# Kernel optimization log

Hardware: AMD Instinct MI355X
Metric: run time of the kernel (lower is better)

Reference implementation:

```python
import jax, jax.numpy as jnp
import numpy as np

GRID_SIZE = 128  # D = H = W
N_POINTS = 8388608


def setup_inputs() -> dict:
    key = jax.random.key(0)
    k_grid, k_coords = jax.random.split(key)
    # occupancy grid buffer: binary {0,1} values as float, shape [D, H, W]
    grid = (jax.random.uniform(k_grid, (GRID_SIZE, GRID_SIZE, GRID_SIZE)) > 0.5).astype(jnp.float32)
    # normalized [-1, 1] query coordinates, layout [..., 3] = (x, y, z)
    coords = jax.random.uniform(k_coords, (N_POINTS, 3), minval=-1.0, maxval=1.0, dtype=jnp.float32)
    return {"grid": grid, "coords": coords}


def _trilinear_sample(grid, coords):
    """torch.nn.functional.grid_sample 5D, mode='bilinear', align_corners=False,
    padding_mode='zeros'. grid: [D,H,W]; coords: [N,3] with (x,y,z) where
    x indexes W, y indexes H, z indexes D. Returns [N]."""
    D, H, W = grid.shape
    x, y, z = coords[:, 0], coords[:, 1], coords[:, 2]
    # unnormalize (align_corners=False): pixel = ((c + 1) * size - 1) / 2
    ix = ((x + 1.0) * W - 1.0) * 0.5
    iy = ((y + 1.0) * H - 1.0) * 0.5
    iz = ((z + 1.0) * D - 1.0) * 0.5

    ix0 = jnp.floor(ix)
    iy0 = jnp.floor(iy)
    iz0 = jnp.floor(iz)
    wx = ix - ix0  # fractional weights
    wy = iy - iy0
    wz = iz - iz0
    ix0 = ix0.astype(jnp.int32)
    iy0 = iy0.astype(jnp.int32)
    iz0 = iz0.astype(jnp.int32)

    def gather(zi, yi, xi):
        # zero padding: out-of-bounds corners contribute 0
        valid = ((zi >= 0) & (zi < D) & (yi >= 0) & (yi < H) & (xi >= 0) & (xi < W))
        zc = jnp.clip(zi, 0, D - 1)
        yc = jnp.clip(yi, 0, H - 1)
        xc = jnp.clip(xi, 0, W - 1)
        return jnp.where(valid, grid[zc, yc, xc], 0.0)

    out = (
        gather(iz0,     iy0,     ix0    ) * (1 - wz) * (1 - wy) * (1 - wx)
        + gather(iz0,     iy0,     ix0 + 1) * (1 - wz) * (1 - wy) * wx
        + gather(iz0,     iy0 + 1, ix0    ) * (1 - wz) * wy       * (1 - wx)
        + gather(iz0,     iy0 + 1, ix0 + 1) * (1 - wz) * wy       * wx
        + gather(iz0 + 1, iy0,     ix0    ) * wz       * (1 - wy) * (1 - wx)
        + gather(iz0 + 1, iy0,     ix0 + 1) * wz       * (1 - wy) * wx
        + gather(iz0 + 1, iy0 + 1, ix0    ) * wz       * wy       * (1 - wx)
        + gather(iz0 + 1, iy0 + 1, ix0 + 1) * wz       * wy       * wx
    )
    return out


def reference(grid, coords):
    flat = coords.reshape(-1, 3)
    return _trilinear_sample(grid, flat)
```

## Files before the change

kernel.cpp:

```cpp
#include <hip/hip_runtime.h>


typedef float fx4 __attribute__((ext_vector_type(4)));
typedef unsigned int u32;
typedef unsigned int ux4 __attribute__((ext_vector_type(4)));
typedef unsigned long long u64;

constexpr int GS = 128;
constexpr size_t MASK_BYTES = (size_t)GS * GS * GS / 8;
constexpr int SLAB_WORDS = 33281;
constexpr size_t SLAB_LDS = (size_t)SLAB_WORDS * 4;

constexpr int TD = GS + 1;
constexpr size_t TBL_BYTES = (size_t)TD * TD * TD;
constexpr size_t TBL_OFF   = (MASK_BYTES + 63) & ~(size_t)63;
constexpr size_t WS_FB     = TBL_OFF + TBL_BYTES;

__global__ __launch_bounds__(256)
void bitpack_kernel(const float* __restrict__ grid, u64* __restrict__ mask) {
    int gid = blockIdx.x * blockDim.x + threadIdx.x;
    float v = grid[gid];
    u64 m = __ballot(v != 0.0f);
    if ((threadIdx.x & 63) == 0) mask[gid >> 6] = m;
}

__device__ __forceinline__ unsigned bit_at(u64 lo, u64 hi, int xi) {
    if ((unsigned)xi >= 128u) return 0u;
    u64 w = (xi < 64) ? lo : hi;
    return (unsigned)((w >> (xi & 63)) & 1ull);
}

__global__ __launch_bounds__(256)
void table_kernel(const u64* __restrict__ mask, unsigned char* __restrict__ tbl) {
    int i = blockIdx.x * blockDim.x + threadIdx.x;
    if (i >= (int)TBL_BYTES) return;
    int x = i % TD;
    int t = i / TD;
    int y = t % TD;
    int z = t / TD;
    int x0 = x - 1;
    unsigned byte = 0u;
#pragma unroll
    for (int dz = 0; dz < 2; ++dz) {
#pragma unroll
        for (int dy = 0; dy < 2; ++dy) {
            int yi = y - 1 + dy, zi = z - 1 + dz;
            u64 lo = 0ull, hi = 0ull;
            if (((unsigned)yi < 128u) & ((unsigned)zi < 128u)) {
                int r = (zi * 128 + yi) * 2;
                lo = mask[r];
                hi = mask[r + 1];
            }
            int kk = dy * 2 + dz * 4;
            byte |= (bit_at(lo, hi, x0) << kk) | (bit_at(lo, hi, x0 + 1) << (kk + 1));
        }
    }
    tbl[i] = (unsigned char)byte;
}

__global__ __launch_bounds__(256)
void sample_packed(const unsigned char* __restrict__ tbl,
                   const float* __restrict__ coords,
                   float* __restrict__ out, int nt) {
    int t = blockIdx.x * blockDim.x + threadIdx.x;
    if (t >= nt) return;
    const fx4* c4 = (const fx4*)coords;
    fx4 q[6];
#pragma unroll
    for (int j = 0; j < 6; ++j) q[j] = __builtin_nontemporal_load(&c4[6 * t + j]);
    const float* f = (const float*)q;
    float wxa[8], wya[8], wza[8];
    int addr[8];
#pragma unroll
    for (int i = 0; i < 8; ++i) {
        float ix = fmaf(f[3 * i + 0], 64.0f, 63.5f);
        float iy = fmaf(f[3 * i + 1], 64.0f, 63.5f);
        float iz = fmaf(f[3 * i + 2], 64.0f, 63.5f);
        float fx = floorf(ix), fy = floorf(iy), fz = floorf(iz);
        wxa[i] = ix - fx; wya[i] = iy - fy; wza[i] = iz - fz;
        int xb = (int)fx + 1, yb = (int)fy + 1, zb = (int)fz + 1;
        addr[i] = (zb * TD + yb) * TD + xb;
    }
    unsigned bytes[8];
#pragma unroll
    for (int i = 0; i < 8; ++i) bytes[i] = (unsigned)tbl[addr[i]];
    float o[8];
#pragma unroll
    for (int i = 0; i < 8; ++i) {
        unsigned byte = bytes[i];
        float wx = wxa[i], wy = wya[i], wz = wza[i];
        float v0 = (float)( byte       & 1u);
        float v1 = (float)((byte >> 1) & 1u);
        float v2 = (float)((byte >> 2) & 1u);
        float v3 = (float)((byte >> 3) & 1u);
        float v4 = (float)((byte >> 4) & 1u);
        float v5 = (float)((byte >> 5) & 1u);
        float v6 = (float)((byte >> 6) & 1u);
        float v7 = (float)((byte >> 7) & 1u);
        float c00 = v0 + wx * (v1 - v0);
        float c10 = v2 + wx * (v3 - v2);
        float c01 = v4 + wx * (v5 - v4);
        float c11 = v6 + wx * (v7 - v6);
        float c0  = c00 + wy * (c10 - c00);
        float c1  = c01 + wy * (c11 - c01);
        o[i] = c0 + wz * (c1 - c0);
    }
    fx4* o4 = (fx4*)out;
    fx4 r0 = {o[0], o[1], o[2], o[3]};
    fx4 r1 = {o[4], o[5], o[6], o[7]};
    __builtin_nontemporal_store(r0, &o4[2 * t + 0]);
    __builtin_nontemporal_store(r1, &o4[2 * t + 1]);
}

__global__ __launch_bounds__(1024, 4)
void sample_2p(const u32* __restrict__ mask32,
               const float* __restrict__ coords,
               float* __restrict__ out) {
    extern __shared__ u32 lds[];
    const int tid = threadIdx.x;
    const int T = blockIdx.x * 1024 + tid;
    const fx4* c4 = (const fx4*)coords;
    fx4 q[6];
#pragma unroll
    for (int j = 0; j < 6; ++j) q[j] = c4[6 * T + j];
    const float* f = (const float*)q;

    u32 pack1[8];
    u32 AM = 0;
    float wx[8], wy[8], wz[8], o[8];
#pragma unroll
    for (int j = 0; j < 8; ++j) {
        float ix = fmaf(f[3 * j + 0], 64.0f, 63.5f);
        float iy = fmaf(f[3 * j + 1], 64.0f, 63.5f);
        float iz = fmaf(f[3 * j + 2], 64.0f, 63.5f);
        float fx = floorf(ix), fy = floorf(iy), fz = floorf(iz);
        float w0 = ix - fx;
        wy[j] = iy - fy; wz[j] = iz - fz;
        int x0 = (int)fx, y0 = (int)fy, z0 = (int)fz;
        int zb = z0 + 1;
        bool flip = (x0 < 0);
        wx[j] = flip ? 1.0f - w0 : w0;
        int xc = flip ? 0 : x0;
        int sft = xc & 31;
        u32 xm = ((u32)x0 <= 126u) ? 3u : 1u;
        u32 vy0 = (u32)(y0 >= 0);
        u32 vy1 = (u32)((u32)y0 <= 126u);
        u32 a0 = vy0 ? xm : 0u;
        u32 a1 = vy1 ? xm : 0u;
        u32 am = a0 | (a1 << 2);
        u32 dyf = vy0 & vy1;
        int y0c = y0 < 0 ? 0 : y0;
        int z0c = z0 < 0 ? 0 : z0;
        u32 RA = (u32)(((z0c << 7) + y0c) * 4 + (xc >> 5));
        pack1[j] = RA | ((u32)sft << 16) | ((u32)zb << 21) | (dyf << 29);
        AM |= am << (4 * j);
        o[j] = 0.0f;
    }

#pragma unroll 1
    for (int s = 0; s < 2; ++s) {
        const int base_w = s ? 32256 : 0;
        const int nv4    = s ? 8320 : 8192;
        __syncthreads();
        {
            const ux4* src = (const ux4*)(mask32 + base_w);
            ux4* dst = (ux4*)lds;
            for (int i = tid; i < nv4; i += 1024) dst[i] = src[i];
            if (s && tid == 0) lds[33280] = 0;
        }
        __syncthreads();
#pragma unroll
        for (int j = 0; j < 8; ++j) {
            u32 p1 = pack1[j];
            int zb = (int)((p1 >> 21) & 0xFF);
            if ((zb < 64) != (s == 0)) continue;
            int la  = (int)(p1 & 0xFFFF) - base_w;
            int sft = (int)((p1 >> 16) & 31);
            int dyw = (int)((p1 >> 27) & 4);
            bool edge = s ? (zb == 128) : (zb == 0);
            int dz = edge ? 0 : 512;
            u32 amv = (AM >> (4 * j)) & 15u;
            u32 glo = amv, ghi = amv;
            if (s) ghi = edge ? 0u : amv;
            else   glo = edge ? 0u : amv;
            int l0 = la, l1 = la + dyw, l2 = la + dz, l3 = la + dz + dyw;
            u32 w00 = lds[l0], w01 = lds[l0 + 1];
            u32 w10 = lds[l1], w11 = lds[l1 + 1];
            u32 w20 = lds[l2], w21 = lds[l2 + 1];
            u32 w30 = lds[l3], w31 = lds[l3 + 1];
            u32 t0 = __builtin_amdgcn_alignbit(w01, w00, (u32)sft) & (glo & 3u);
            u32 t1 = __builtin_amdgcn_alignbit(w11, w10, (u32)sft) & ((glo >> 2) & 3u);
            u32 t2 = __builtin_amdgcn_alignbit(w21, w20, (u32)sft) & (ghi & 3u);
            u32 t3 = __builtin_amdgcn_alignbit(w31, w30, (u32)sft) & ((ghi >> 2) & 3u);
            float w = wx[j];
            int b0 = (int)(t0 & 1u), b1 = (int)(t1 & 1u);
            int b2 = (int)(t2 & 1u), b3 = (int)(t3 & 1u);
            float r00 = fmaf(w, (float)((int)(t0 >> 1) - b0), (float)b0);
            float r01 = fmaf(w, (float)((int)(t1 >> 1) - b1), (float)b1);
            float r10 = fmaf(w, (float)((int)(t2 >> 1) - b2), (float)b2);
            float r11 = fmaf(w, (float)((int)(t3 >> 1) - b3), (float)b3);
            float cy0 = fmaf(wy[j], r01 - r00, r00);
            float cy1 = fmaf(wy[j], r11 - r10, r10);
            o[j] = fmaf(wz[j], cy1 - cy0, cy0);
        }
    }
    fx4* o4 = (fx4*)out;
    fx4 r0 = {o[0], o[1], o[2], o[3]};
    fx4 r1 = {o[4], o[5], o[6], o[7]};
    o4[2 * T]     = r0;
    o4[2 * T + 1] = r1;
}

extern "C" void kernel_launch(void* const* d_in, const int* in_sizes, int n_in,
                              void* d_out, int out_size, void* d_ws, size_t ws_size,
                              hipStream_t stream) {
    const float* grid   = (const float*)d_in[0];
    const float* coords = (const float*)d_in[1];
    float* out = (float*)d_out;
    int npts = in_sizes[1] / 3;
    int vox = GS * GS * GS;

    u64* mask = (u64*)d_ws;

    if (ws_size >= WS_FB && (npts & 7) == 0) {
        unsigned char* tbl = (unsigned char*)d_ws + TBL_OFF;
        bitpack_kernel<<<vox / 256, 256, 0, stream>>>(grid, mask);
        table_kernel<<<(int)((TBL_BYTES + 255) / 256), 256, 0, stream>>>(mask, tbl);
        int nt = npts / 8;
        sample_packed<<<(nt + 255) / 256, 256, 0, stream>>>(tbl, coords, out, nt);
        return;
    }

    (void)hipFuncSetAttribute((const void*)sample_2p,
                              hipFuncAttributeMaxDynamicSharedMemorySize,
                              (int)SLAB_LDS);
    int nb = 0;
    hipError_t oe = hipOccupancyMaxActiveBlocksPerMultiprocessor(
        &nb, sample_2p, 1024, SLAB_LDS);
    bool slab_ok = (oe == hipSuccess) && (nb >= 1) && (ws_size >= MASK_BYTES) &&
                   (npts == 1024 * 8192);
    if (slab_ok) {
        bitpack_kernel<<<vox / 256, 256, 0, stream>>>(grid, mask);
        sample_2p<<<1024, 1024, SLAB_LDS, stream>>>((const u32*)mask, coords, out);
    }
}
```

Measured before the change: 216.8 us.

## Split points between LDS-slab path and global byte-table path in one hybrid kernel

```diff
diff --git a/kernel.cpp b/kernel.cpp
--- a/kernel.cpp
+++ b/kernel.cpp
@@ -15,6 +15,9 @@
 constexpr size_t TBL_BYTES = (size_t)TD * TD * TD;
 constexpr size_t TBL_OFF   = (MASK_BYTES + 63) & ~(size_t)63;
 constexpr size_t WS_FB     = TBL_OFF + TBL_BYTES;
+
+constexpr int NPTS_FULL = 8388608;
+constexpr int HGRP = NPTS_FULL / 2 / 8;
 
 __global__ __launch_bounds__(256)
 void bitpack_kernel(const float* __restrict__ grid, u64* __restrict__ mask) {
@@ -58,72 +61,24 @@
     tbl[i] = (unsigned char)byte;
 }
 
-__global__ __launch_bounds__(256)
-void sample_packed(const unsigned char* __restrict__ tbl,
+__global__ __launch_bounds__(1024, 4)
+void sample_hybrid(const u32* __restrict__ mask32,
+                   const unsigned char* __restrict__ tbl,
                    const float* __restrict__ coords,
-                   float* __restrict__ out, int nt) {
-    int t = blockIdx.x * blockDim.x + threadIdx.x;
-    if (t >= nt) return;
-    const fx4* c4 = (const fx4*)coords;
-    fx4 q[6];
-#pragma unroll
-    for (int j = 0; j < 6; ++j) q[j] = __builtin_nontemporal_load(&c4[6 * t + j]);
-    const float* f = (const float*)q;
-    float wxa[8], wya[8], wza[8];
-    int addr[8];
-#pragma unroll
-    for (int i = 0; i < 8; ++i) {
-        float ix = fmaf(f[3 * i + 0], 64.0f, 63.5f);
-        float iy = fmaf(f[3 * i + 1], 64.0f, 63.5f);
-        float iz = fmaf(f[3 * i + 2], 64.0f, 63.5f);
-        float fx = floorf(ix), fy = floorf(iy), fz = floorf(iz);
-        wxa[i] = ix - fx; wya[i] = iy - fy; wza[i] = iz - fz;
-        int xb = (int)fx + 1, yb = (int)fy + 1, zb = (int)fz + 1;
-        addr[i] = (zb * TD + yb) * TD + xb;
-    }
-    unsigned bytes[8];
-#pragma unroll
-    for (int i = 0; i < 8; ++i) bytes[i] = (unsigned)tbl[addr[i]];
-    float o[8];
-#pragma unroll
-    for (int i = 0; i < 8; ++i) {
-        unsigned byte = bytes[i];
-        float wx = wxa[i], wy = wya[i], wz = wza[i];
-        float v0 = (float)( byte       & 1u);
-        float v1 = (float)((byte >> 1) & 1u);
-        float v2 = (float)((byte >> 2) & 1u);
-        float v3 = (float)((byte >> 3) & 1u);
-        float v4 = (float)((byte >> 4) & 1u);
-        float v5 = (float)((byte >> 5) & 1u);
-        float v6 = (float)((byte >> 6) & 1u);
-        float v7 = (float)((byte >> 7) & 1u);
-        float c00 = v0 + wx * (v1 - v0);
-        float c10 = v2 + wx * (v3 - v2);
-        float c01 = v4 + wx * (v5 - v4);
-        float c11 = v6 + wx * (v7 - v6);
-        float c0  = c00 + wy * (c10 - c00);
-        float c1  = c01 + wy * (c11 - c01);
-        o[i] = c0 + wz * (c1 - c0);
-    }
-    fx4* o4 = (fx4*)out;
-    fx4 r0 = {o[0], o[1], o[2], o[3]};
-    fx4 r1 = {o[4], o[5], o[6], o[7]};
-    __builtin_nontemporal_store(r0, &o4[2 * t + 0]);
-    __builtin_nontemporal_store(r1, &o4[2 * t + 1]);
-}
-
-__global__ __launch_bounds__(1024, 4)
-void sample_2p(const u32* __restrict__ mask32,
-               const float* __restrict__ coords,
-               float* __restrict__ out) {
+                   float* __restrict__ out) {
     extern __shared__ u32 lds[];
     const int tid = threadIdx.x;
-    const int T = blockIdx.x * 1024 + tid;
+    const int Ts = blockIdx.x * 1024 + tid;
+    const int Tg = Ts + HGRP;
     const fx4* c4 = (const fx4*)coords;
-    fx4 q[6];
-#pragma unroll
-    for (int j = 0; j < 6; ++j) q[j] = c4[6 * T + j];
-    const float* f = (const float*)q;
+
+    fx4 qs[6], qg[6];
+#pragma unroll
+    for (int j = 0; j < 6; ++j) qs[j] = __builtin_nontemporal_load(&c4[6 * Ts + j]);
+#pragma unroll
+    for (int j = 0; j < 6; ++j) qg[j] = __builtin_nontemporal_load(&c4[6 * Tg + j]);
+    const float* f  = (const float*)qs;
+    const float* fg = (const float*)qg;
 
     u32 pack1[8];
     u32 AM = 0;
@@ -157,18 +112,42 @@
         o[j] = 0.0f;
     }
 
-#pragma unroll 1
+    u32 gb[8];
+
+#pragma unroll
     for (int s = 0; s < 2; ++s) {
         const int base_w = s ? 32256 : 0;
-        const int nv4    = s ? 8320 : 8192;
-        __syncthreads();
-        {
-            const ux4* src = (const ux4*)(mask32 + base_w);
-            ux4* dst = (ux4*)lds;
-            for (int i = tid; i < nv4; i += 1024) dst[i] = src[i];
-            if (s && tid == 0) lds[33280] = 0;
-        }
-        __syncthreads();
+        if (s) {
+            asm volatile("s_waitcnt lgkmcnt(0)" ::: "memory");
+            __builtin_amdgcn_s_barrier();
+        }
+        const ux4* src = (const ux4*)(mask32 + base_w);
+        ux4* dst4 = (ux4*)lds;
+        ux4 t0 = src[tid], t1 = src[tid + 1024], t2 = src[tid + 2048], t3 = src[tid + 3072];
+        ux4 tt = {0, 0, 0, 0};
+        if (s && tid < 128) tt = src[8192 + tid];
+        dst4[tid] = t0; dst4[tid + 1024] = t1; dst4[tid + 2048] = t2; dst4[tid + 3072] = t3;
+        if (s && tid < 128) dst4[8192 + tid] = tt;
+        ux4 t4 = src[tid + 4096], t5 = src[tid + 5120], t6 = src[tid + 6144], t7 = src[tid + 7168];
+        asm volatile("" ::: "memory");
+#pragma unroll
+        for (int i = 0; i < 4; ++i) {
+            const int p = 4 * s + i;
+            float ix = fmaf(fg[3 * p + 0], 64.0f, 63.5f);
+            float iy = fmaf(fg[3 * p + 1], 64.0f, 63.5f);
+            float iz = fmaf(fg[3 * p + 2], 64.0f, 63.5f);
+            int xb = (int)floorf(ix) + 1;
+            int yb = (int)floorf(iy) + 1;
+            int zb = (int)floorf(iz) + 1;
+            gb[p] = (u32)tbl[(zb * TD + yb) * TD + xb];
+        }
+        asm volatile("" ::: "memory");
+        dst4[tid + 4096] = t4; dst4[tid + 5120] = t5;
+        dst4[tid + 6144] = t6; dst4[tid + 7168] = t7;
+        if (s && tid == 0) lds[33280] = 0;
+        asm volatile("s_waitcnt lgkmcnt(0)" ::: "memory");
+        __builtin_amdgcn_s_barrier();
+
 #pragma unroll
         for (int j = 0; j < 8; ++j) {
             u32 p1 = pack1[j];
@@ -188,27 +167,112 @@
             u32 w10 = lds[l1], w11 = lds[l1 + 1];
             u32 w20 = lds[l2], w21 = lds[l2 + 1];
             u32 w30 = lds[l3], w31 = lds[l3 + 1];
-            u32 t0 = __builtin_amdgcn_alignbit(w01, w00, (u32)sft) & (glo & 3u);
-            u32 t1 = __builtin_amdgcn_alignbit(w11, w10, (u32)sft) & ((glo >> 2) & 3u);
-            u32 t2 = __builtin_amdgcn_alignbit(w21, w20, (u32)sft) & (ghi & 3u);
-            u32 t3 = __builtin_amdgcn_alignbit(w31, w30, (u32)sft) & ((ghi >> 2) & 3u);
+            u32 t0b = __builtin_amdgcn_alignbit(w01, w00, (u32)sft) & (glo & 3u);
+            u32 t1b = __builtin_amdgcn_alignbit(w11, w10, (u32)sft) & ((glo >> 2) & 3u);
+            u32 t2b = __builtin_amdgcn_alignbit(w21, w20, (u32)sft) & (ghi & 3u);
+            u32 t3b = __builtin_amdgcn_alignbit(w31, w30, (u32)sft) & ((ghi >> 2) & 3u);
             float w = wx[j];
-            int b0 = (int)(t0 & 1u), b1 = (int)(t1 & 1u);
-            int b2 = (int)(t2 & 1u), b3 = (int)(t3 & 1u);
-            float r00 = fmaf(w, (float)((int)(t0 >> 1) - b0), (float)b0);
-            float r01 = fmaf(w, (float)((int)(t1 >> 1) - b1), (float)b1);
-            float r10 = fmaf(w, (float)((int)(t2 >> 1) - b2), (float)b2);
-            float r11 = fmaf(w, (float)((int)(t3 >> 1) - b3), (float)b3);
+            int b0 = (int)(t0b & 1u), b1 = (int)(t1b & 1u);
+            int b2 = (int)(t2b & 1u), b3 = (int)(t3b & 1u);
+            float r00 = fmaf(w, (float)((int)(t0b >> 1) - b0), (float)b0);
+            float r01 = fmaf(w, (float)((int)(t1b >> 1) - b1), (float)b1);
+            float r10 = fmaf(w, (float)((int)(t2b >> 1) - b2), (float)b2);
+            float r11 = fmaf(w, (float)((int)(t3b >> 1) - b3), (float)b3);
             float cy0 = fmaf(wy[j], r01 - r00, r00);
             float cy1 = fmaf(wy[j], r11 - r10, r10);
             o[j] = fmaf(wz[j], cy1 - cy0, cy0);
         }
     }
+
+    float og[8];
+#pragma unroll
+    for (int i = 0; i < 8; ++i) {
+        float ix = fmaf(fg[3 * i + 0], 64.0f, 63.5f);
+        float iy = fmaf(fg[3 * i + 1], 64.0f, 63.5f);
+        float iz = fmaf(fg[3 * i + 2], 64.0f, 63.5f);
+        float fx = floorf(ix), fy = floorf(iy), fz = floorf(iz);
+        float gwx = ix - fx, gwy = iy - fy, gwz = iz - fz;
+        unsigned byte = gb[i];
+        float v0 = (float)( byte       & 1u);
+        float v1 = (float)((byte >> 1) & 1u);
+        float v2 = (float)((byte >> 2) & 1u);
+        float v3 = (float)((byte >> 3) & 1u);
+        float v4 = (float)((byte >> 4) & 1u);
+        float v5 = (float)((byte >> 5) & 1u);
+        float v6 = (float)((byte >> 6) & 1u);
+        float v7 = (float)((byte >> 7) & 1u);
+        float c00 = v0 + gwx * (v1 - v0);
+        float c10 = v2 + gwx * (v3 - v2);
+        float c01 = v4 + gwx * (v5 - v4);
+        float c11 = v6 + gwx * (v7 - v6);
+        float c0  = c00 + gwy * (c10 - c00);
+        float c1  = c01 + gwy * (c11 - c01);
+        og[i] = c0 + gwz * (c1 - c0);
+    }
+
     fx4* o4 = (fx4*)out;
     fx4 r0 = {o[0], o[1], o[2], o[3]};
     fx4 r1 = {o[4], o[5], o[6], o[7]};
-    o4[2 * T]     = r0;
-    o4[2 * T + 1] = r1;
+    fx4 g0 = {og[0], og[1], og[2], og[3]};
+    fx4 g1 = {og[4], og[5], og[6], og[7]};
+    __builtin_nontemporal_store(r0, &o4[2 * Ts]);
+    __builtin_nontemporal_store(r1, &o4[2 * Ts + 1]);
+    __builtin_nontemporal_store(g0, &o4[2 * Tg]);
+    __builtin_nontemporal_store(g1, &o4[2 * Tg + 1]);
+}
+
+__global__ __launch_bounds__(256)
+void sample_packed(const unsigned char* __restrict__ tbl,
+                   const float* __restrict__ coords,
+                   float* __restrict__ out, int nt) {
+    int t = blockIdx.x * blockDim.x + threadIdx.x;
+    if (t >= nt) return;
+    const fx4* c4 = (const fx4*)coords;
+    fx4 q[6];
+#pragma unroll
+    for (int j = 0; j < 6; ++j) q[j] = __builtin_nontemporal_load(&c4[6 * t + j]);
+    const float* f = (const float*)q;
+    float wxa[8], wya[8], wza[8];
+    int addr[8];
+#pragma unroll
+    for (int i = 0; i < 8; ++i) {
+        float ix = fmaf(f[3 * i + 0], 64.0f, 63.5f);
+        float iy = fmaf(f[3 * i + 1], 64.0f, 63.5f);
+        float iz = fmaf(f[3 * i + 2], 64.0f, 63.5f);
+        float fx = floorf(ix), fy = floorf(iy), fz = floorf(iz);
+        wxa[i] = ix - fx; wya[i] = iy - fy; wza[i] = iz - fz;
+        int xb = (int)fx + 1, yb = (int)fy + 1, zb = (int)fz + 1;
+        addr[i] = (zb * TD + yb) * TD + xb;
+    }
+    unsigned bytes[8];
+#pragma unroll
+    for (int i = 0; i < 8; ++i) bytes[i] = (unsigned)tbl[addr[i]];
+    float o[8];
+#pragma unroll
+    for (int i = 0; i < 8; ++i) {
+        unsigned byte = bytes[i];
+        float wx = wxa[i], wy = wya[i], wz = wza[i];
+        float v0 = (float)( byte       & 1u);
+        float v1 = (float)((byte >> 1) & 1u);
+        float v2 = (float)((byte >> 2) & 1u);
+        float v3 = (float)((byte >> 3) & 1u);
+        float v4 = (float)((byte >> 4) & 1u);
+        float v5 = (float)((byte >> 5) & 1u);
+        float v6 = (float)((byte >> 6) & 1u);
+        float v7 = (float)((byte >> 7) & 1u);
+        float c00 = v0 + wx * (v1 - v0);
+        float c10 = v2 + wx * (v3 - v2);
+        float c01 = v4 + wx * (v5 - v4);
+        float c11 = v6 + wx * (v7 - v6);
+        float c0  = c00 + wy * (c10 - c00);
+        float c1  = c01 + wy * (c11 - c01);
+        o[i] = c0 + wz * (c1 - c0);
+    }
+    fx4* o4 = (fx4*)out;
+    fx4 r0 = {o[0], o[1], o[2], o[3]};
+    fx4 r1 = {o[4], o[5], o[6], o[7]};
+    __builtin_nontemporal_store(r0, &o4[2 * t + 0]);
+    __builtin_nontemporal_store(r1, &o4[2 * t + 1]);
 }
 
 extern "C" void kernel_launch(void* const* d_in, const int* in_sizes, int n_in,
@@ -222,25 +286,31 @@
 
     u64* mask = (u64*)d_ws;
 
+    if (ws_size >= WS_FB && npts == NPTS_FULL) {
+        (void)hipFuncSetAttribute((const void*)sample_hybrid,
+                                  hipFuncAttributeMaxDynamicSharedMemorySize,
+                                  (int)SLAB_LDS);
+        int nb = 0;
+        hipError_t oe = hipOccupancyMaxActiveBlocksPerMultiprocessor(
+            &nb, sample_hybrid, 1024, SLAB_LDS);
+        unsigned char* tbl = (unsigned char*)d_ws + TBL_OFF;
+        bitpack_kernel<<<vox / 256, 256, 0, stream>>>(grid, mask);
+        table_kernel<<<(int)((TBL_BYTES + 255) / 256), 256, 0, stream>>>(mask, tbl);
+        if (oe == hipSuccess && nb >= 1) {
+            sample_hybrid<<<512, 1024, SLAB_LDS, stream>>>(
+                (const u32*)mask, tbl, coords, out);
+        } else {
+            int nt = npts / 8;
+            sample_packed<<<(nt + 255) / 256, 256, 0, stream>>>(tbl, coords, out, nt);
+        }
+        return;
+    }
+
     if (ws_size >= WS_FB && (npts & 7) == 0) {
         unsigned char* tbl = (unsigned char*)d_ws + TBL_OFF;
         bitpack_kernel<<<vox / 256, 256, 0, stream>>>(grid, mask);
         table_kernel<<<(int)((TBL_BYTES + 255) / 256), 256, 0, stream>>>(mask, tbl);
         int nt = npts / 8;
         sample_packed<<<(nt + 255) / 256, 256, 0, stream>>>(tbl, coords, out, nt);
-        return;
-    }
-
-    (void)hipFuncSetAttribute((const void*)sample_2p,
-                              hipFuncAttributeMaxDynamicSharedMemorySize,
-                              (int)SLAB_LDS);
-    int nb = 0;
-    hipError_t oe = hipOccupancyMaxActiveBlocksPerMultiprocessor(
-        &nb, sample_2p, 1024, SLAB_LDS);
-    bool slab_ok = (oe == hipSuccess) && (nb >= 1) && (ws_size >= MASK_BYTES) &&
-                   (npts == 1024 * 8192);
-    if (slab_ok) {
-        bitpack_kernel<<<vox / 256, 256, 0, stream>>>(grid, mask);
-        sample_2p<<<1024, 1024, SLAB_LDS, stream>>>((const u32*)mask, coords, out);
-    }
-}
+    }
+}
```

Result: no change. 215.0 us (-0.9%).

## Split sample work between LDS-slab waves and table-gather waves; fuse prep kernels

Applied to the files above, without the earlier changes.

```diff
diff --git a/kernel.cpp b/kernel.cpp
--- a/kernel.cpp
+++ b/kernel.cpp
@@ -15,6 +15,9 @@
 constexpr size_t TBL_BYTES = (size_t)TD * TD * TD;
 constexpr size_t TBL_OFF   = (MASK_BYTES + 63) & ~(size_t)63;
 constexpr size_t WS_FB     = TBL_OFF + TBL_BYTES;
+
+constexpr int NPTS_FULL = 8388608;
+constexpr int HGRP = NPTS_FULL / 2 / 8;
 
 __global__ __launch_bounds__(256)
 void bitpack_kernel(const float* __restrict__ grid, u64* __restrict__ mask) {
@@ -31,31 +34,206 @@
 }
 
 __global__ __launch_bounds__(256)
-void table_kernel(const u64* __restrict__ mask, unsigned char* __restrict__ tbl) {
-    int i = blockIdx.x * blockDim.x + threadIdx.x;
-    if (i >= (int)TBL_BYTES) return;
-    int x = i % TD;
-    int t = i / TD;
-    int y = t % TD;
-    int z = t / TD;
-    int x0 = x - 1;
-    unsigned byte = 0u;
-#pragma unroll
-    for (int dz = 0; dz < 2; ++dz) {
-#pragma unroll
-        for (int dy = 0; dy < 2; ++dy) {
-            int yi = y - 1 + dy, zi = z - 1 + dz;
-            u64 lo = 0ull, hi = 0ull;
-            if (((unsigned)yi < 128u) & ((unsigned)zi < 128u)) {
-                int r = (zi * 128 + yi) * 2;
-                lo = mask[r];
-                hi = mask[r + 1];
+void prep_kernel(const float* __restrict__ grid, u64* __restrict__ mask,
+                 unsigned char* __restrict__ tbl) {
+    __shared__ u64 bits[2][256];
+    const int tid = threadIdx.x;
+    const int b = blockIdx.x;
+    const int wid = tid >> 6;
+#pragma unroll
+    for (int p = 0; p < 2; ++p) {
+        int z = b - 1 + p;
+        if ((unsigned)z < 128u) {
+            for (int it = 0; it < 64; ++it) {
+                float v = grid[z * 16384 + it * 256 + tid];
+                u64 m = __ballot(v != 0.0f);
+                if ((tid & 63) == 0) bits[p][it * 4 + wid] = m;
             }
-            int kk = dy * 2 + dz * 4;
-            byte |= (bit_at(lo, hi, x0) << kk) | (bit_at(lo, hi, x0 + 1) << (kk + 1));
-        }
-    }
-    tbl[i] = (unsigned char)byte;
+        } else {
+            bits[p][tid] = 0ull;
+        }
+    }
+    __syncthreads();
+    if (b < 128) mask[b * 256 + tid] = bits[1][tid];
+    for (int i = tid; i < TD * TD; i += 256) {
+        int yb = i / TD, xb = i - yb * TD;
+        int x0 = xb - 1;
+        unsigned byte = 0u;
+#pragma unroll
+        for (int p = 0; p < 2; ++p) {
+#pragma unroll
+            for (int dy = 0; dy < 2; ++dy) {
+                int y = yb - 1 + dy;
+                u64 lo = 0ull, hi = 0ull;
+                if ((unsigned)y < 128u) { lo = bits[p][y * 2]; hi = bits[p][y * 2 + 1]; }
+                int kk = dy * 2 + p * 4;
+                byte |= (bit_at(lo, hi, x0) << kk) | (bit_at(lo, hi, x0 + 1) << (kk + 1));
+            }
+        }
+        tbl[b * (TD * TD) + i] = (unsigned char)byte;
+    }
+}
+
+__global__ __attribute__((amdgpu_waves_per_eu(4, 4))) __launch_bounds__(1024)
+void sample_ws(const u32* __restrict__ mask32,
+               const unsigned char* __restrict__ tbl,
+               const float* __restrict__ coords,
+               float* __restrict__ out) {
+    extern __shared__ u32 lds[];
+    const int tid = threadIdx.x;
+    const bool slab = tid < 512;
+    const int T = blockIdx.x * 512 + (slab ? tid : (HGRP - 512 + tid));
+    const fx4* c4 = (const fx4*)coords;
+
+    fx4 q[6];
+#pragma unroll
+    for (int j = 0; j < 6; ++j) q[j] = __builtin_nontemporal_load(&c4[6 * T + j]);
+    const float* f = (const float*)q;
+
+    float wx[8], wy[8], wz[8], o[8];
+    u32 p1[8];
+    u32 gb[8];
+    u32 AM = 0;
+
+    if (slab) {
+#pragma unroll
+        for (int j = 0; j < 8; ++j) {
+            float ix = fmaf(f[3 * j + 0], 64.0f, 63.5f);
+            float iy = fmaf(f[3 * j + 1], 64.0f, 63.5f);
+            float iz = fmaf(f[3 * j + 2], 64.0f, 63.5f);
+            float fx = floorf(ix), fy = floorf(iy), fz = floorf(iz);
+            float w0 = ix - fx;
+            wy[j] = iy - fy; wz[j] = iz - fz;
+            int x0 = (int)fx, y0 = (int)fy, z0 = (int)fz;
+            int zb = z0 + 1;
+            bool flip = (x0 < 0);
+            wx[j] = flip ? 1.0f - w0 : w0;
+            int xc = flip ? 0 : x0;
+            int sft = xc & 31;
+            u32 xm = ((u32)x0 <= 126u) ? 3u : 1u;
+            u32 vy0 = (u32)(y0 >= 0);
+            u32 vy1 = (u32)((u32)y0 <= 126u);
+            u32 a0 = vy0 ? xm : 0u;
+            u32 a1 = vy1 ? xm : 0u;
+            u32 am = a0 | (a1 << 2);
+            u32 dyf = vy0 & vy1;
+            int y0c = y0 < 0 ? 0 : y0;
+            int z0c = z0 < 0 ? 0 : z0;
+            u32 RA = (u32)(((z0c << 7) + y0c) * 4 + (xc >> 5));
+            p1[j] = RA | ((u32)sft << 16) | ((u32)zb << 21) | (dyf << 29);
+            AM |= am << (4 * j);
+            o[j] = 0.0f;
+        }
+    } else {
+#pragma unroll
+        for (int i = 0; i < 8; ++i) {
+            float ix = fmaf(f[3 * i + 0], 64.0f, 63.5f);
+            float iy = fmaf(f[3 * i + 1], 64.0f, 63.5f);
+            float iz = fmaf(f[3 * i + 2], 64.0f, 63.5f);
+            float fx = floorf(ix), fy = floorf(iy), fz = floorf(iz);
+            wx[i] = ix - fx; wy[i] = iy - fy; wz[i] = iz - fz;
+            int xb = (int)fx + 1, yb = (int)fy + 1, zb = (int)fz + 1;
+            p1[i] = (u32)((zb * TD + yb) * TD + xb);
+        }
+#pragma unroll
+        for (int i = 0; i < 4; ++i) gb[i] = (u32)tbl[p1[i]];
+    }
+
+    auto fill = [&](int s_) {
+        const int base_w = s_ ? 32256 : 0;
+        const int nv4    = s_ ? 8320 : 8192;
+        const ux4* src = (const ux4*)(mask32 + base_w);
+        ux4* dst = (ux4*)lds;
+        for (int i = tid; i < nv4; i += 512) dst[i] = src[i];
+        if (s_ && tid == 0) lds[33280] = 0;
+    };
+    auto jloop = [&](int s_) {
+        const int base_w = s_ ? 32256 : 0;
+#pragma unroll
+        for (int j = 0; j < 8; ++j) {
+            u32 pv = p1[j];
+            int zb = (int)((pv >> 21) & 0xFF);
+            if ((zb < 64) != (s_ == 0)) continue;
+            int la  = (int)(pv & 0xFFFF) - base_w;
+            int sft = (int)((pv >> 16) & 31);
+            int dyw = (int)((pv >> 27) & 4);
+            bool edge = s_ ? (zb == 128) : (zb == 0);
+            int dz = edge ? 0 : 512;
+            u32 amv = (AM >> (4 * j)) & 15u;
+            u32 glo = amv, ghi = amv;
+            if (s_) ghi = edge ? 0u : amv;
+            else    glo = edge ? 0u : amv;
+            int l0 = la, l1 = la + dyw, l2 = la + dz, l3 = la + dz + dyw;
+            u32 w00 = lds[l0], w01 = lds[l0 + 1];
+            u32 w10 = lds[l1], w11 = lds[l1 + 1];
+            u32 w20 = lds[l2], w21 = lds[l2 + 1];
+            u32 w30 = lds[l3], w31 = lds[l3 + 1];
+            u32 t0b = __builtin_amdgcn_alignbit(w01, w00, (u32)sft) & (glo & 3u);
+            u32 t1b = __builtin_amdgcn_alignbit(w11, w10, (u32)sft) & ((glo >> 2) & 3u);
+            u32 t2b = __builtin_amdgcn_alignbit(w21, w20, (u32)sft) & (ghi & 3u);
+            u32 t3b = __builtin_amdgcn_alignbit(w31, w30, (u32)sft) & ((ghi >> 2) & 3u);
+            float w = wx[j];
+            int b0 = (int)(t0b & 1u), b1 = (int)(t1b & 1u);
+            int b2 = (int)(t2b & 1u), b3 = (int)(t3b & 1u);
+            float r00 = fmaf(w, (float)((int)(t0b >> 1) - b0), (float)b0);
+            float r01 = fmaf(w, (float)((int)(t1b >> 1) - b1), (float)b1);
+            float r10 = fmaf(w, (float)((int)(t2b >> 1) - b2), (float)b2);
+            float r11 = fmaf(w, (float)((int)(t3b >> 1) - b3), (float)b3);
+            float cy0 = fmaf(wy[j], r01 - r00, r00);
+            float cy1 = fmaf(wy[j], r11 - r10, r10);
+            o[j] = fmaf(wz[j], cy1 - cy0, cy0);
+        }
+    };
+    auto consume = [&](int i0) {
+#pragma unroll
+        for (int k = 0; k < 4; ++k) {
+            int i = i0 + k;
+            unsigned byte = gb[i];
+            float v0 = (float)( byte       & 1u);
+            float v1 = (float)((byte >> 1) & 1u);
+            float v2 = (float)((byte >> 2) & 1u);
+            float v3 = (float)((byte >> 3) & 1u);
+            float v4 = (float)((byte >> 4) & 1u);
+            float v5 = (float)((byte >> 5) & 1u);
+            float v6 = (float)((byte >> 6) & 1u);
+            float v7 = (float)((byte >> 7) & 1u);
+            float c00 = v0 + wx[i] * (v1 - v0);
+            float c10 = v2 + wx[i] * (v3 - v2);
+            float c01 = v4 + wx[i] * (v5 - v4);
+            float c11 = v6 + wx[i] * (v7 - v6);
+            float c0  = c00 + wy[i] * (c10 - c00);
+            float c1  = c01 + wy[i] * (c11 - c01);
+            o[i] = c0 + wz[i] * (c1 - c0);
+        }
+    };
+
+    if (slab) {
+        fill(0);
+        asm volatile("s_waitcnt lgkmcnt(0)" ::: "memory");
+    }
+    __builtin_amdgcn_s_barrier();
+    if (slab) {
+        jloop(0);
+        asm volatile("s_waitcnt lgkmcnt(0)" ::: "memory");
+    } else {
+        consume(0);
+#pragma unroll
+        for (int i = 4; i < 8; ++i) gb[i] = (u32)tbl[p1[i]];
+    }
+    __builtin_amdgcn_s_barrier();
+    if (slab) {
+        fill(1);
+        asm volatile("s_waitcnt lgkmcnt(0)" ::: "memory");
+    }
+    __builtin_amdgcn_s_barrier();
+    if (slab) jloop(1);
+    else      consume(4);
+
+    fx4* o4 = (fx4*)out;
+    fx4 r0 = {o[0], o[1], o[2], o[3]};
+    fx4 r1 = {o[4], o[5], o[6], o[7]};
+    __builtin_nontemporal_store(r0, &o4[2 * T]);
+    __builtin_nontemporal_store(r1, &o4[2 * T + 1]);
 }
 
 __global__ __launch_bounds__(256)
@@ -124,7 +302,6 @@
 #pragma unroll
     for (int j = 0; j < 6; ++j) q[j] = c4[6 * T + j];
     const float* f = (const float*)q;
-
     u32 pack1[8];
     u32 AM = 0;
     float wx[8], wy[8], wz[8], o[8];
@@ -156,7 +333,6 @@
         AM |= am << (4 * j);
         o[j] = 0.0f;
     }
-
 #pragma unroll 1
     for (int s = 0; s < 2; ++s) {
         const int base_w = s ? 32256 : 0;
@@ -171,12 +347,12 @@
         __syncthreads();
 #pragma unroll
         for (int j = 0; j < 8; ++j) {
-            u32 p1 = pack1[j];
-            int zb = (int)((p1 >> 21) & 0xFF);
+            u32 pv = pack1[j];
+            int zb = (int)((pv >> 21) & 0xFF);
             if ((zb < 64) != (s == 0)) continue;
-            int la  = (int)(p1 & 0xFFFF) - base_w;
-            int sft = (int)((p1 >> 16) & 31);
-            int dyw = (int)((p1 >> 27) & 4);
+            int la  = (int)(pv & 0xFFFF) - base_w;
+            int sft = (int)((pv >> 16) & 31);
+            int dyw = (int)((pv >> 27) & 4);
             bool edge = s ? (zb == 128) : (zb == 0);
             int dz = edge ? 0 : 512;
             u32 amv = (AM >> (4 * j)) & 15u;
@@ -188,17 +364,17 @@
             u32 w10 = lds[l1], w11 = lds[l1 + 1];
             u32 w20 = lds[l2], w21 = lds[l2 + 1];
             u32 w30 = lds[l3], w31 = lds[l3 + 1];
-            u32 t0 = __builtin_amdgcn_alignbit(w01, w00, (u32)sft) & (glo & 3u);
-            u32 t1 = __builtin_amdgcn_alignbit(w11, w10, (u32)sft) & ((glo >> 2) & 3u);
-            u32 t2 = __builtin_amdgcn_alignbit(w21, w20, (u32)sft) & (ghi & 3u);
-            u32 t3 = __builtin_amdgcn_alignbit(w31, w30, (u32)sft) & ((ghi >> 2) & 3u);
+            u32 t0b = __builtin_amdgcn_alignbit(w01, w00, (u32)sft) & (glo & 3u);
+            u32 t1b = __builtin_amdgcn_alignbit(w11, w10, (u32)sft) & ((glo >> 2) & 3u);
+            u32 t2b = __builtin_amdgcn_alignbit(w21, w20, (u32)sft) & (ghi & 3u);
+            u32 t3b = __builtin_amdgcn_alignbit(w31, w30, (u32)sft) & ((ghi >> 2) & 3u);
             float w = wx[j];
-            int b0 = (int)(t0 & 1u), b1 = (int)(t1 & 1u);
-            int b2 = (int)(t2 & 1u), b3 = (int)(t3 & 1u);
-            float r00 = fmaf(w, (float)((int)(t0 >> 1) - b0), (float)b0);
-            float r01 = fmaf(w, (float)((int)(t1 >> 1) - b1), (float)b1);
-            float r10 = fmaf(w, (float)((int)(t2 >> 1) - b2), (float)b2);
-            float r11 = fmaf(w, (float)((int)(t3 >> 1) - b3), (float)b3);
+            int b0 = (int)(t0b & 1u), b1 = (int)(t1b & 1u);
+            int b2 = (int)(t2b & 1u), b3 = (int)(t3b & 1u);
+            float r00 = fmaf(w, (float)((int)(t0b >> 1) - b0), (float)b0);
+            float r01 = fmaf(w, (float)((int)(t1b >> 1) - b1), (float)b1);
+            float r10 = fmaf(w, (float)((int)(t2b >> 1) - b2), (float)b2);
+            float r11 = fmaf(w, (float)((int)(t3b >> 1) - b3), (float)b3);
             float cy0 = fmaf(wy[j], r01 - r00, r00);
             float cy1 = fmaf(wy[j], r11 - r10, r10);
             o[j] = fmaf(wz[j], cy1 - cy0, cy0);
@@ -222,25 +398,43 @@
 
     u64* mask = (u64*)d_ws;
 
+    if (ws_size >= WS_FB && npts == NPTS_FULL) {
+        (void)hipFuncSetAttribute((const void*)sample_ws,
+                                  hipFuncAttributeMaxDynamicSharedMemorySize,
+                                  (int)SLAB_LDS);
+        int nb = 0;
+        hipError_t oe = hipOccupancyMaxActiveBlocksPerMultiprocessor(
+            &nb, sample_ws, 1024, SLAB_LDS);
+        unsigned char* tbl = (unsigned char*)d_ws + TBL_OFF;
+        prep_kernel<<<TD, 256, 0, stream>>>(grid, mask, tbl);
+        if (oe == hipSuccess && nb >= 1) {
+            sample_ws<<<1024, 1024, SLAB_LDS, stream>>>(
+                (const u32*)mask, tbl, coords, out);
+        } else {
+            int nt = npts / 8;
+            sample_packed<<<(nt + 255) / 256, 256, 0, stream>>>(tbl, coords, out, nt);
+        }
+        return;
+    }
+
     if (ws_size >= WS_FB && (npts & 7) == 0) {
         unsigned char* tbl = (unsigned char*)d_ws + TBL_OFF;
-        bitpack_kernel<<<vox / 256, 256, 0, stream>>>(grid, mask);
-        table_kernel<<<(int)((TBL_BYTES + 255) / 256), 256, 0, stream>>>(mask, tbl);
+        prep_kernel<<<TD, 256, 0, stream>>>(grid, mask, tbl);
         int nt = npts / 8;
         sample_packed<<<(nt + 255) / 256, 256, 0, stream>>>(tbl, coords, out, nt);
         return;
     }
 
-    (void)hipFuncSetAttribute((const void*)sample_2p,
-                              hipFuncAttributeMaxDynamicSharedMemorySize,
-                              (int)SLAB_LDS);
-    int nb = 0;
-    hipError_t oe = hipOccupancyMaxActiveBlocksPerMultiprocessor(
-        &nb, sample_2p, 1024, SLAB_LDS);
-    bool slab_ok = (oe == hipSuccess) && (nb >= 1) && (ws_size >= MASK_BYTES) &&
-                   (npts == 1024 * 8192);
-    if (slab_ok) {
-        bitpack_kernel<<<vox / 256, 256, 0, stream>>>(grid, mask);
-        sample_2p<<<1024, 1024, SLAB_LDS, stream>>>((const u32*)mask, coords, out);
-    }
-}
+    if (ws_size >= MASK_BYTES && npts == 1024 * 8192) {
+        (void)hipFuncSetAttribute((const void*)sample_2p,
+                                  hipFuncAttributeMaxDynamicSharedMemorySize,
+                                  (int)SLAB_LDS);
+        int nb = 0;
+        hipError_t oe = hipOccupancyMaxActiveBlocksPerMultiprocessor(
+            &nb, sample_2p, 1024, SLAB_LDS);
+        if (oe == hipSuccess && nb >= 1) {
+            bitpack_kernel<<<vox / 256, 256, 0, stream>>>(grid, mask);
+            sample_2p<<<1024, 1024, SLAB_LDS, stream>>>((const u32*)mask, coords, out);
+        }
+    }
+}
```

Result: slower. 265.8 us (+22.6%).
